# Kernel optimization log

Hardware: AMD Instinct MI355X
Metric: run time of the kernel (lower is better)

## Reference

```python
import jax, jax.numpy as jnp
import numpy as np

L = 160        # voxel grid side
BATCH = 4
N_SAMPLE = 62500
N = 64


def _build_coords():
    rng = np.random.default_rng(0)
    coords = []
    for b in range(BATCH):
        c = np.unique(rng.integers(0, L, (N_SAMPLE, 3)), axis=0)  # sorted, unique
        bc = np.concatenate([np.full((len(c), 1), b, dtype=np.int64), c.astype(np.int64)], axis=1)
        coords.append(bc)
    return np.concatenate(coords, axis=0)  # [P,4] = (batch, x, y, z), globally key-sorted


def _neighbor_table(C):
    # integer key per coordinate; coords are unique+sorted so keys are strictly increasing
    keys = ((C[:, 0] * L + C[:, 1]) * L + C[:, 2]) * L + C[:, 3]
    P = C.shape[0]
    offs = np.array([[dx, dy, dz] for dx in (-1, 0, 1) for dy in (-1, 0, 1) for dz in (-1, 0, 1)], dtype=np.int64)
    nbr = np.full((P, 27), -1, dtype=np.int32)
    for k, o in enumerate(offs):
        nc = C[:, 1:] + o
        valid = np.all((nc >= 0) & (nc < L), axis=1)
        nk = ((C[:, 0] * L + nc[:, 0]) * L + nc[:, 1]) * L + nc[:, 2]
        pos = np.clip(np.searchsorted(keys, nk), 0, P - 1)
        found = valid & (keys[pos] == nk)
        nbr[:, k] = np.where(found, pos, -1).astype(np.int32)
    return nbr


def setup_inputs() -> dict:
    C = _build_coords()
    nbr = _neighbor_table(C)
    P = C.shape[0]
    key = jax.random.key(0)
    ks = jax.random.split(key, 10)
    s = 0.05  # small weight scale keeps activations well-conditioned
    return {
        "feats": jax.random.normal(ks[0], (P, N), jnp.float32),
        "cond": jax.random.normal(ks[1], (P, 2 * N), jnp.float32),
        "W1a": jax.random.normal(ks[2], (27, N, N), jnp.float32) * s,
        "b1a": jax.random.normal(ks[3], (N,), jnp.float32) * s,
        "W1b": jax.random.normal(ks[4], (27, N, N), jnp.float32) * s,
        "b1b": jax.random.normal(ks[5], (N,), jnp.float32) * s,
        "W2a": jax.random.normal(ks[6], (27, N, N), jnp.float32) * s,
        "b2a": jax.random.normal(ks[7], (N,), jnp.float32) * s,
        "W2b": jax.random.normal(ks[8], (27, N, N), jnp.float32) * s,
        "b2b": jax.random.normal(ks[9], (N,), jnp.float32) * s,
        "nbr": jnp.asarray(nbr),
    }


def _sparse_conv(x, nbr, W, b):
    # x: [P,N] features, nbr: [P,27] neighbor indices (-1 = missing)
    mask = (nbr >= 0)
    idx = jnp.maximum(nbr, 0)
    acc0 = jnp.zeros((x.shape[0], W.shape[2]), x.dtype)

    def body(acc, kin):
        wk, ik, mk = kin            # wk:[N,N], ik:[P], mk:[P]
        g = x[ik] * mk[:, None].astype(x.dtype)
        return acc + g @ wk, None

    out, _ = jax.lax.scan(body, acc0, (W, idx.T, mask.T))
    return out + b


def reference(feats, cond, W1a, b1a, W1b, b1b, W2a, b2a, W2b, b2b, nbr):
    x_res = feats
    # conv_1: conv -> relu -> conv
    h = _sparse_conv(feats, nbr, W1a, b1a)
    h = jax.nn.relu(h)
    h = _sparse_conv(h, nbr, W1b, b1b)
    # FiLM from condition (features_at_coordinates at identical coords -> direct lookup)
    beta, gamma = jnp.split(cond, 2, axis=1)
    h = h * beta + gamma
    # conv_2: conv -> relu -> conv -> relu
    h = _sparse_conv(h, nbr, W2a, b2a)
    h = jax.nn.relu(h)
    h = _sparse_conv(h, nbr, W2b, b2b)
    h = jax.nn.relu(h)
    # residual: x_res at same coordinates is an identity lookup
    return h + x_res
```

## Files before the change

kernel.cpp:

```cpp
#include <hip/hip_runtime.h>
#include <hip/hip_bf16.h>


#define N 64
#define TAPS 27
#define MT 128

typedef unsigned short u16;
typedef __attribute__((ext_vector_type(8))) short short8;
typedef __attribute__((ext_vector_type(16))) float floatx16;

__device__ __forceinline__ float bf2f(u16 v) {
    union { unsigned u; float f; } c;
    c.u = ((unsigned)v) << 16;
    return c.f;
}
__device__ __forceinline__ u16 f2bf(float f) {
    __hip_bfloat16 h = __float2bfloat16(f);
    u16 r;
    __builtin_memcpy(&r, &h, 2);
    return r;
}
__device__ __forceinline__ void split2(float x, u16& hi, u16& lo) {
    hi = f2bf(x);
    lo = f2bf(x - bf2f(hi));
}

__global__ void split_feats(const float* __restrict__ x, u16* __restrict__ hl, int n) {
    int i = blockIdx.x * 256 + threadIdx.x;
    if (i >= n) return;
    int p = i >> 6, c = i & 63;
    u16 h, l;
    split2(x[i], h, l);
    hl[(size_t)p * 128 + c] = h;
    hl[(size_t)p * 128 + 64 + c] = l;
}

__global__ void transpose_w(const float* __restrict__ W, u16* __restrict__ Wt) {
    const float* src = W + blockIdx.x * (N * N);
    u16* dst = Wt + blockIdx.x * (N * 128);
    int t = threadIdx.x;
#pragma unroll
    for (int m = 0; m < 16; ++m) {
        int e = t + m * 256;
        int i = e >> 6;
        int j = e & 63;
        u16 h, l;
        split2(src[e], h, l);
        dst[j * 128 + i] = h;
        dst[j * 128 + 64 + i] = l;
    }
}

template <int MODE>
__global__ __launch_bounds__(256, 3) void conv_k(
    const u16* __restrict__ Xhl, const u16* __restrict__ Wt,
    const float* __restrict__ bias, const int* __restrict__ nbr,
    const float* __restrict__ cond, const float* __restrict__ resid,
    u16* __restrict__ out_hl, float* __restrict__ out_f32, int P) {
    __shared__ u16 Ah[MT * 64];
    __shared__ u16 Al[MT * 64];
    __shared__ u16 Bh[N * 64];
    __shared__ u16 Bl[N * 64];

    const int tid = threadIdx.x;
    const int pbase = blockIdx.x * MT;

    const int ar = tid >> 1;
    const int ahalf = tid & 1;
    const int br = tid >> 2;
    const int bq = tid & 3;

    const int w = tid >> 6;
    const int lane = tid & 63;
    const int cn = lane & 31;
    const int kh = lane >> 5;

    floatx16 acc[2];
#pragma unroll
    for (int nt = 0; nt < 2; ++nt)
#pragma unroll
        for (int i = 0; i < 16; ++i) acc[nt][i] = 0.f;

    const int prA = pbase + ar;
    const long nbrbase = (long)prA * TAPS;
    int idx = (prA < P) ? nbr[nbrbase] : -1;

    const u16* wrow0 = Wt + (size_t)br * 128;

    for (int k = 0; k < TAPS; ++k) {
        if (k) __syncthreads();

        {
            const u16* xrow = Xhl + (size_t)idx * 128;
#pragma unroll
            for (int c = 0; c < 4; ++c) {
                int g = 4 * ahalf + c;
                int gs = (g ^ (ar & 7)) * 8;
                uint4 vh = make_uint4(0u, 0u, 0u, 0u);
                uint4 vl = make_uint4(0u, 0u, 0u, 0u);
                if (idx >= 0) {
                    vh = *reinterpret_cast<const uint4*>(xrow + g * 8);
                    vl = *reinterpret_cast<const uint4*>(xrow + 64 + g * 8);
                }
                *reinterpret_cast<uint4*>(&Ah[ar * 64 + gs]) = vh;
                *reinterpret_cast<uint4*>(&Al[ar * 64 + gs]) = vl;
            }
        }
        {
            const u16* wrow = wrow0 + (size_t)k * (N * 128);
#pragma unroll
            for (int jg = 0; jg < 2; ++jg) {
                int g = bq + 4 * jg;
                int gs = (g ^ (br & 7)) * 8;
                *reinterpret_cast<uint4*>(&Bh[br * 64 + gs]) =
                    *reinterpret_cast<const uint4*>(wrow + g * 8);
                *reinterpret_cast<uint4*>(&Bl[br * 64 + gs]) =
                    *reinterpret_cast<const uint4*>(wrow + 64 + g * 8);
            }
        }
        idx = (k + 1 < TAPS && prA < P) ? nbr[nbrbase + k + 1] : -1;

        __syncthreads();

        const int rowA = w * 32 + cn;
#pragma unroll
        for (int kc = 0; kc < 4; ++kc) {
            int g = 2 * kc + kh;
            int offA = rowA * 64 + ((g ^ (rowA & 7)) * 8);
            short8 a_h = *reinterpret_cast<const short8*>(&Ah[offA]);
            short8 a_l = *reinterpret_cast<const short8*>(&Al[offA]);
#pragma unroll
            for (int nt = 0; nt < 2; ++nt) {
                int j = nt * 32 + cn;
                int offB = j * 64 + ((g ^ (j & 7)) * 8);
                short8 b_h = *reinterpret_cast<const short8*>(&Bh[offB]);
                short8 b_l = *reinterpret_cast<const short8*>(&Bl[offB]);
                acc[nt] = __builtin_amdgcn_mfma_f32_32x32x16_bf16(a_h, b_h, acc[nt], 0, 0, 0);
                acc[nt] = __builtin_amdgcn_mfma_f32_32x32x16_bf16(a_h, b_l, acc[nt], 0, 0, 0);
                acc[nt] = __builtin_amdgcn_mfma_f32_32x32x16_bf16(a_l, b_h, acc[nt], 0, 0, 0);
            }
        }
    }

#pragma unroll
    for (int nt = 0; nt < 2; ++nt) {
        int j = nt * 32 + cn;
        float bj = bias[j];
#pragma unroll
        for (int reg = 0; reg < 16; ++reg) {
            int row = (reg & 3) + 8 * (reg >> 2) + 4 * kh;
            int p = pbase + w * 32 + row;
            if (p < P) {
                float o = acc[nt][reg] + bj;
                if (MODE == 0 || MODE == 2) o = fmaxf(o, 0.f);
                if (MODE == 1) {
                    float be = cond[(size_t)p * (2 * N) + j];
                    float ga = cond[(size_t)p * (2 * N) + N + j];
                    o = o * be + ga;
                }
                if (MODE == 3) {
                    o = fmaxf(o, 0.f) + resid[(size_t)p * N + j];
                    out_f32[(size_t)p * N + j] = o;
                } else {
                    u16 h, l;
                    split2(o, h, l);
                    out_hl[(size_t)p * 128 + j] = h;
                    out_hl[(size_t)p * 128 + 64 + j] = l;
                }
            }
        }
    }
}

extern "C" void kernel_launch(void* const* d_in, const int* in_sizes, int n_in,
                              void* d_out, int out_size, void* d_ws, size_t ws_size,
                              hipStream_t stream) {
    const float* feats = (const float*)d_in[0];
    const float* cond  = (const float*)d_in[1];
    const float* W1a   = (const float*)d_in[2];
    const float* b1a   = (const float*)d_in[3];
    const float* W1b   = (const float*)d_in[4];
    const float* b1b   = (const float*)d_in[5];
    const float* W2a   = (const float*)d_in[6];
    const float* b2a   = (const float*)d_in[7];
    const float* W2b   = (const float*)d_in[8];
    const float* b2b   = (const float*)d_in[9];
    const int* nbr     = (const int*)d_in[10];
    float* out = (float*)d_out;
    u16* out_hl = (u16*)d_out;

    const int P = in_sizes[0] / N;

    const size_t wtElems = (size_t)TAPS * N * 128;
    u16* wt0 = (u16*)d_ws;
    u16* wt1 = wt0 + wtElems;
    u16* wt2 = wt1 + wtElems;
    u16* wt3 = wt2 + wtElems;
    u16* hA  = wt3 + wtElems;

    transpose_w<<<TAPS, 256, 0, stream>>>(W1a, wt0);
    transpose_w<<<TAPS, 256, 0, stream>>>(W1b, wt1);
    transpose_w<<<TAPS, 256, 0, stream>>>(W2a, wt2);
    transpose_w<<<TAPS, 256, 0, stream>>>(W2b, wt3);
    split_feats<<<(P * N + 255) / 256, 256, 0, stream>>>(feats, out_hl, P * N);

    const int blocks = (P + MT - 1) / MT;
    conv_k<0><<<blocks, 256, 0, stream>>>(out_hl, wt0, b1a, nbr, nullptr, nullptr, hA, nullptr, P);
    conv_k<1><<<blocks, 256, 0, stream>>>(hA, wt1, b1b, nbr, cond, nullptr, out_hl, nullptr, P);
    conv_k<2><<<blocks, 256, 0, stream>>>(out_hl, wt2, b2a, nbr, nullptr, nullptr, hA, nullptr, P);
    conv_k<3><<<blocks, 256, 0, stream>>>(hA, wt3, b2b, nbr, nullptr, feats, nullptr, out, P);
}
```

Before: 1.069 ms.

## Double the conv M-tile and prefetch next tap's gathers into registers

The conv kernel's row tile grows from 128 to 256 points, so each wave computes a 64x64 output block with four accumulators. Each B fragment loaded from LDS is reused across two A row tiles, and the weight tile is loaded once per 256 points instead of once per 128. The next tap's neighbor gather and weight tile are loaded into registers while the current tap's MFMAs run, then written to a single LDS buffer after a barrier, hiding gather latency behind compute. In exchange, register use rises sharply (16+4 uint4 staging registers plus four accumulators), occupancy drops to 2 blocks per CU, and there are half as many blocks to spread across CUs.

```diff
diff --git a/kernel.cpp b/kernel.cpp
--- a/kernel.cpp
+++ b/kernel.cpp
@@ -4,7 +4,7 @@
 
 #define N 64
 #define TAPS 27
-#define MT 128
+#define MT 256
 
 typedef unsigned short u16;
 typedef __attribute__((ext_vector_type(8))) short short8;
@@ -53,110 +53,131 @@
 }
 
 template <int MODE>
-__global__ __launch_bounds__(256, 3) void conv_k(
+__global__ __launch_bounds__(256, 2) void conv_k(
     const u16* __restrict__ Xhl, const u16* __restrict__ Wt,
     const float* __restrict__ bias, const int* __restrict__ nbr,
     const float* __restrict__ cond, const float* __restrict__ resid,
     u16* __restrict__ out_hl, float* __restrict__ out_f32, int P) {
-    __shared__ u16 Ah[MT * 64];
-    __shared__ u16 Al[MT * 64];
-    __shared__ u16 Bh[N * 64];
-    __shared__ u16 Bl[N * 64];
+    __shared__ __align__(16) u16 As[MT * 128];
+    __shared__ __align__(16) u16 Bs[N * 128];
 
     const int tid = threadIdx.x;
     const int pbase = blockIdx.x * MT;
 
-    const int ar = tid >> 1;
-    const int ahalf = tid & 1;
-    const int br = tid >> 2;
-    const int bq = tid & 3;
+    const int tA = tid;
+    const int prA = pbase + tA;
+    const long nbrbase = (long)prA * TAPS;
+    const int rB = tid >> 2;
+    const int mB = tid & 3;
 
     const int w = tid >> 6;
     const int lane = tid & 63;
     const int cn = lane & 31;
     const int kh = lane >> 5;
-
-    floatx16 acc[2];
-#pragma unroll
-    for (int nt = 0; nt < 2; ++nt)
-#pragma unroll
-        for (int i = 0; i < 16; ++i) acc[nt][i] = 0.f;
-
-    const int prA = pbase + ar;
-    const long nbrbase = (long)prA * TAPS;
-    int idx = (prA < P) ? nbr[nbrbase] : -1;
-
-    const u16* wrow0 = Wt + (size_t)br * 128;
+    const int rowA0 = w * 64 + cn;
+
+    floatx16 acc00, acc01, acc10, acc11;
+#pragma unroll
+    for (int i = 0; i < 16; ++i) { acc00[i] = 0.f; acc01[i] = 0.f; acc10[i] = 0.f; acc11[i] = 0.f; }
+
+    uint4 ra[16];
+    uint4 rb[4];
+
+    int idxN = (prA < P) ? nbr[nbrbase] : -1;
+
+    const u16* wtap = Wt + (size_t)rB * 128;
+
+    auto load_regs = [&](int kload) {
+        const bool valid = (idxN >= 0);
+        const size_t xb = (size_t)(valid ? idxN : 0) * 128;
+#pragma unroll
+        for (int c = 0; c < 16; ++c) {
+            const int s = (c + tA) & 15;
+            const int src = (s >> 3) * 64 + (((s & 7) ^ (tA & 7)) * 8);
+            uint4 v = make_uint4(0u, 0u, 0u, 0u);
+            if (valid) v = *reinterpret_cast<const uint4*>(Xhl + xb + src);
+            ra[c] = v;
+        }
+        const u16* wrow = wtap + (size_t)kload * (N * 128);
+#pragma unroll
+        for (int q = 0; q < 4; ++q) {
+            const int s = (mB + 4 * q + rB) & 15;
+            const int src = (s >> 3) * 64 + (((s & 7) ^ (rB & 7)) * 8);
+            rb[q] = *reinterpret_cast<const uint4*>(wrow + src);
+        }
+        idxN = (kload + 1 < TAPS && prA < P) ? nbr[nbrbase + kload + 1] : -1;
+    };
+
+    auto write_lds = [&]() {
+#pragma unroll
+        for (int c = 0; c < 16; ++c) {
+            const int s = (c + tA) & 15;
+            *reinterpret_cast<uint4*>(&As[tA * 128 + s * 8]) = ra[c];
+        }
+#pragma unroll
+        for (int q = 0; q < 4; ++q) {
+            const int s = (mB + 4 * q + rB) & 15;
+            *reinterpret_cast<uint4*>(&Bs[rB * 128 + s * 8]) = rb[q];
+        }
+    };
+
+    load_regs(0);
+    write_lds();
+    __syncthreads();
 
     for (int k = 0; k < TAPS; ++k) {
-        if (k) __syncthreads();
-
-        {
-            const u16* xrow = Xhl + (size_t)idx * 128;
-#pragma unroll
-            for (int c = 0; c < 4; ++c) {
-                int g = 4 * ahalf + c;
-                int gs = (g ^ (ar & 7)) * 8;
-                uint4 vh = make_uint4(0u, 0u, 0u, 0u);
-                uint4 vl = make_uint4(0u, 0u, 0u, 0u);
-                if (idx >= 0) {
-                    vh = *reinterpret_cast<const uint4*>(xrow + g * 8);
-                    vl = *reinterpret_cast<const uint4*>(xrow + 64 + g * 8);
-                }
-                *reinterpret_cast<uint4*>(&Ah[ar * 64 + gs]) = vh;
-                *reinterpret_cast<uint4*>(&Al[ar * 64 + gs]) = vl;
-            }
-        }
-        {
-            const u16* wrow = wrow0 + (size_t)k * (N * 128);
-#pragma unroll
-            for (int jg = 0; jg < 2; ++jg) {
-                int g = bq + 4 * jg;
-                int gs = (g ^ (br & 7)) * 8;
-                *reinterpret_cast<uint4*>(&Bh[br * 64 + gs]) =
-                    *reinterpret_cast<const uint4*>(wrow + g * 8);
-                *reinterpret_cast<uint4*>(&Bl[br * 64 + gs]) =
-                    *reinterpret_cast<const uint4*>(wrow + 64 + g * 8);
-            }
-        }
-        idx = (k + 1 < TAPS && prA < P) ? nbr[nbrbase + k + 1] : -1;
+        if (k + 1 < TAPS) load_regs(k + 1);
+
+#pragma unroll
+        for (int kc = 0; kc < 4; ++kc) {
+            const int g = 2 * kc + kh;
+            const int sw = (g ^ (cn & 7)) * 8;
+            const short8 a_h0 = *reinterpret_cast<const short8*>(&As[rowA0 * 128 + sw]);
+            const short8 a_l0 = *reinterpret_cast<const short8*>(&As[rowA0 * 128 + 64 + sw]);
+            const short8 a_h1 = *reinterpret_cast<const short8*>(&As[(rowA0 + 32) * 128 + sw]);
+            const short8 a_l1 = *reinterpret_cast<const short8*>(&As[(rowA0 + 32) * 128 + 64 + sw]);
+            const short8 b_h0 = *reinterpret_cast<const short8*>(&Bs[cn * 128 + sw]);
+            const short8 b_l0 = *reinterpret_cast<const short8*>(&Bs[cn * 128 + 64 + sw]);
+            const short8 b_h1 = *reinterpret_cast<const short8*>(&Bs[(cn + 32) * 128 + sw]);
+            const short8 b_l1 = *reinterpret_cast<const short8*>(&Bs[(cn + 32) * 128 + 64 + sw]);
+
+            acc00 = __builtin_amdgcn_mfma_f32_32x32x16_bf16(a_h0, b_h0, acc00, 0, 0, 0);
+            acc00 = __builtin_amdgcn_mfma_f32_32x32x16_bf16(a_h0, b_l0, acc00, 0, 0, 0);
+            acc00 = __builtin_amdgcn_mfma_f32_32x32x16_bf16(a_l0, b_h0, acc00, 0, 0, 0);
+
+            acc01 = __builtin_amdgcn_mfma_f32_32x32x16_bf16(a_h0, b_h1, acc01, 0, 0, 0);
+            acc01 = __builtin_amdgcn_mfma_f32_32x32x16_bf16(a_h0, b_l1, acc01, 0, 0, 0);
+            acc01 = __builtin_amdgcn_mfma_f32_32x32x16_bf16(a_l0, b_h1, acc01, 0, 0, 0);
+
+            acc10 = __builtin_amdgcn_mfma_f32_32x32x16_bf16(a_h1, b_h0, acc10, 0, 0, 0);
+            acc10 = __builtin_amdgcn_mfma_f32_32x32x16_bf16(a_h1, b_l0, acc10, 0, 0, 0);
+            acc10 = __builtin_amdgcn_mfma_f32_32x32x16_bf16(a_l1, b_h0, acc10, 0, 0, 0);
+
+            acc11 = __builtin_amdgcn_mfma_f32_32x32x16_bf16(a_h1, b_h1, acc11, 0, 0, 0);
+            acc11 = __builtin_amdgcn_mfma_f32_32x32x16_bf16(a_h1, b_l1, acc11, 0, 0, 0);
+            acc11 = __builtin_amdgcn_mfma_f32_32x32x16_bf16(a_l1, b_h1, acc11, 0, 0, 0);
+        }
 
         __syncthreads();
-
-        const int rowA = w * 32 + cn;
-#pragma unroll
-        for (int kc = 0; kc < 4; ++kc) {
-            int g = 2 * kc + kh;
-            int offA = rowA * 64 + ((g ^ (rowA & 7)) * 8);
-            short8 a_h = *reinterpret_cast<const short8*>(&Ah[offA]);
-            short8 a_l = *reinterpret_cast<const short8*>(&Al[offA]);
-#pragma unroll
-            for (int nt = 0; nt < 2; ++nt) {
-                int j = nt * 32 + cn;
-                int offB = j * 64 + ((g ^ (j & 7)) * 8);
-                short8 b_h = *reinterpret_cast<const short8*>(&Bh[offB]);
-                short8 b_l = *reinterpret_cast<const short8*>(&Bl[offB]);
-                acc[nt] = __builtin_amdgcn_mfma_f32_32x32x16_bf16(a_h, b_h, acc[nt], 0, 0, 0);
-                acc[nt] = __builtin_amdgcn_mfma_f32_32x32x16_bf16(a_h, b_l, acc[nt], 0, 0, 0);
-                acc[nt] = __builtin_amdgcn_mfma_f32_32x32x16_bf16(a_l, b_h, acc[nt], 0, 0, 0);
-            }
+        if (k + 1 < TAPS) {
+            write_lds();
+            __syncthreads();
         }
     }
 
-#pragma unroll
-    for (int nt = 0; nt < 2; ++nt) {
-        int j = nt * 32 + cn;
-        float bj = bias[j];
+    auto epi = [&](const floatx16& a, int mt, int nt) {
+        const int j = nt * 32 + cn;
+        const float bj = bias[j];
 #pragma unroll
         for (int reg = 0; reg < 16; ++reg) {
-            int row = (reg & 3) + 8 * (reg >> 2) + 4 * kh;
-            int p = pbase + w * 32 + row;
+            const int row = (reg & 3) + 8 * (reg >> 2) + 4 * kh;
+            const int p = pbase + w * 64 + mt * 32 + row;
             if (p < P) {
-                float o = acc[nt][reg] + bj;
+                float o = a[reg] + bj;
                 if (MODE == 0 || MODE == 2) o = fmaxf(o, 0.f);
                 if (MODE == 1) {
-                    float be = cond[(size_t)p * (2 * N) + j];
-                    float ga = cond[(size_t)p * (2 * N) + N + j];
+                    const float be = cond[(size_t)p * (2 * N) + j];
+                    const float ga = cond[(size_t)p * (2 * N) + N + j];
                     o = o * be + ga;
                 }
                 if (MODE == 3) {
@@ -170,7 +191,11 @@
                 }
             }
         }
-    }
+    };
+    epi(acc00, 0, 0);
+    epi(acc01, 0, 1);
+    epi(acc10, 1, 0);
+    epi(acc11, 1, 1);
 }
 
 extern "C" void kernel_launch(void* const* d_in, const int* in_sizes, int n_in,
```

Result: slower. 1.318 ms (+23.4%).
